# Optimization experiments

Hardware: AMD Instinct MI355X
Metric: run time of the kernel (lower is better)

Reference implementation:

```python
import jax, jax.numpy as jnp
import numpy as np

DIM = 70      # voxel grid side
NE = 6        # element channels
B = 8         # batch
TARGET = 29   # TARGET_NUM in source


def _xavier(key, shape, fan_in, fan_out):
    lim = float(np.sqrt(6.0 / (fan_in + fan_out)))
    return jax.random.uniform(key, shape, jnp.float32, -lim, lim)


def setup_inputs() -> dict:
    key = jax.random.key(0)
    ks = jax.random.split(key, 12)
    # Sparse binary occupancy grid: ~34 atoms per channel per molecule.
    x = (jax.random.uniform(ks[0], (B, NE, DIM, DIM, DIM)) < 1e-4).astype(jnp.float32)
    sigma = 2.0 * jnp.ones((NE,), jnp.float32)
    k3 = 3 * 3 * 3
    conv1_w = _xavier(ks[1], (32, NE, 3, 3, 3), NE * k3, 32 * k3)
    conv2_w = _xavier(ks[2], (64, 32, 3, 3, 3), 32 * k3, 64 * k3)
    conv3_w = _xavier(ks[3], (128, 64, 3, 3, 3), 64 * k3, 128 * k3)
    conv4_w = _xavier(ks[4], (256, 128, 3, 3, 3), 128 * k3, 256 * k3)
    conv1_b = jnp.full((32,), 0.01, jnp.float32)
    conv2_b = jnp.full((64,), 0.01, jnp.float32)
    conv3_b = jnp.full((128,), 0.01, jnp.float32)
    conv4_b = jnp.full((256,), 0.01, jnp.float32)
    fc1_w = _xavier(ks[5], (1024, 2048), 2048, 1024)
    fc1_b = jnp.full((1024,), 0.01, jnp.float32)
    fc2_w = _xavier(ks[6], (TARGET, 1024), 1024, TARGET)
    fc2_b = jax.random.uniform(ks[7], (TARGET,), jnp.float32, -1.0 / 32.0, 1.0 / 32.0)
    return dict(x=x, sigma=sigma,
                conv1_w=conv1_w, conv1_b=conv1_b, conv2_w=conv2_w, conv2_b=conv2_b,
                conv3_w=conv3_w, conv3_b=conv3_b, conv4_w=conv4_w, conv4_b=conv4_b,
                fc1_w=fc1_w, fc1_b=fc1_b, fc2_w=fc2_w, fc2_b=fc2_b)


def _blur(x, sigma):
    # Faithful to source: Gaussian centered at raw voxel INDICES (x0,y0,z0 from
    # nonzero()) but evaluated on SHIFTED coords arange(-dim/2, dim/2).
    # Separable Gaussian -> three 1D contractions instead of per-atom loops.
    coords = jnp.arange(DIM, dtype=jnp.float32) - DIM / 2.0   # -35 .. 34
    idx = jnp.arange(DIM, dtype=jnp.float32)                   # 0 .. 69
    d2 = (coords[:, None] - idx[None, :]) ** 2                 # [70,70]
    G = jnp.exp(-d2[None, :, :] / (2.0 * sigma[:, None, None] ** 2))  # [e,out,in]
    mask = (x != 0).astype(x.dtype)                            # [b,e,i,j,k]
    t = jnp.einsum('beijk,eai->beajk', mask, G)
    t = jnp.einsum('beajk,epj->beapk', t, G)
    cube = jnp.einsum('beapk,eqk->beapq', t, G)                # [b,e,70,70,70]
    return cube


def _conv3d(h, w, b):
    y = jax.lax.conv_general_dilated(h, w, (1, 1, 1), 'VALID',
                                     dimension_numbers=('NCDHW', 'OIDHW', 'NCDHW'))
    return y + b[None, :, None, None, None]


def _pool(h):
    return jax.lax.reduce_window(h, -jnp.inf, jax.lax.max,
                                 (1, 1, 2, 2, 2), (1, 1, 2, 2, 2), 'VALID')


def reference(x, sigma, conv1_w, conv1_b, conv2_w, conv2_b, conv3_w, conv3_b,
              conv4_w, conv4_b, fc1_w, fc1_b, fc2_w, fc2_b):
    h = _blur(x, sigma)
    h = jax.nn.relu(_pool(_conv3d(h, conv1_w, conv1_b)))
    h = jax.nn.relu(_pool(_conv3d(h, conv2_w, conv2_b)))
    h = jax.nn.relu(_pool(_conv3d(h, conv3_w, conv3_b)))
    h = jax.nn.relu(_pool(_conv3d(h, conv4_w, conv4_b)))  # [B,256,2,2,2]
    v = h.reshape(x.shape[0], -1)                          # [B,2048]
    y1 = jax.nn.relu(v @ fc1_w.T + fc1_b)
    y2 = y1 @ fc2_w.T + fc2_b                              # [B,29]
    return y2
```

## Files before the change

### kernel.cpp

```cpp
#include <hip/hip_runtime.h>
#include <hip/hip_bf16.h>

#define DIMV 70
#define NEL 6
#define BATCH 8

typedef unsigned short u16;
typedef unsigned int u32;
typedef __bf16 bf16x8 __attribute__((ext_vector_type(8)));
typedef short short8v __attribute__((ext_vector_type(8)));
typedef float f32x4 __attribute__((ext_vector_type(4)));

__device__ __forceinline__ u16 f2bf(float f) {
  __hip_bfloat16 h = __float2bfloat16(f);
  return __builtin_bit_cast(u16, h);
}
__device__ __forceinline__ float bf2f(u16 u) {
  unsigned int x = ((unsigned int)u) << 16;
  return __builtin_bit_cast(float, x);
}

__global__ __launch_bounds__(256) void k_zero(float* __restrict__ p, int n4) {
  int i = blockIdx.x * 256 + threadIdx.x;
  if (i < n4) ((float4*)p)[i] = make_float4(0.f, 0.f, 0.f, 0.f);
}

__global__ __launch_bounds__(256) void k_scan(const float* __restrict__ x,
                                              int* __restrict__ cnt,
                                              int* __restrict__ lists) {
  const int N4 = (BATCH * NEL * DIMV * DIMV * DIMV) / 4;
  int i = blockIdx.x * 256 + threadIdx.x;
  if (i >= N4) return;
  float4 v = ((const float4*)x)[i];
  int ch = i / 85750;
  int local = 4 * i - ch * 343000;
  float f[4] = {v.x, v.y, v.z, v.w};
#pragma unroll
  for (int k = 0; k < 4; ++k) {
    if (f[k] != 0.f) {
      int slot = atomicAdd(&cnt[ch], 1);
      if (slot < 512) lists[ch * 512 + slot] = local + k;
    }
  }
}

__global__ __launch_bounds__(256) void k_gather(const int* __restrict__ cnt,
                                                const int* __restrict__ lists,
                                                const float* __restrict__ sigma,
                                                u32* __restrict__ cube, int b0) {
  const int z = blockIdx.x;
  const int bl = blockIdx.y / NEL;
  const int e = blockIdx.y % NEL;
  const int chG = (b0 + bl) * NEL + e;
  const int tid = threadIdx.x;
  float sg = sigma[e];
  float inv2s2 = 1.f / (2.f * sg * sg);

  __shared__ int s_n;
  __shared__ int s_idx[512];
  __shared__ float s_wz[512];
  __shared__ float s_wy[32 * 70];
  __shared__ float s_wx[32 * 70];

  if (tid == 0) s_n = 0;
  __syncthreads();
  int n = min(cnt[chG], 512);
  for (int t = tid; t < n; t += 256) {
    int idx = lists[chG * 512 + t];
    int i0 = idx / 4900;
    float d = (float)(z - 35 - i0);
    float wz = expf(-d * d * inv2s2);
    if (wz > 1e-30f) {
      int s = atomicAdd(&s_n, 1);
      s_idx[s] = idx;
      s_wz[s] = wz;
    }
  }
  __syncthreads();
  int m = s_n;

  float acc[20];
#pragma unroll
  for (int k = 0; k < 20; ++k) acc[k] = 0.f;

  for (int t0 = 0; t0 < m; t0 += 32) {
    int tn = min(32, m - t0);
    __syncthreads();
    for (int u = tid; u < tn * 70; u += 256) {
      int t = u / 70, pos = u % 70;
      int idx = s_idx[t0 + t];
      int j0 = (idx / 70) % 70, k0 = idx % 70;
      float dy = (float)(pos - 35 - j0);
      float dx = (float)(pos - 35 - k0);
      s_wy[t * 70 + pos] = s_wz[t0 + t] * expf(-dy * dy * inv2s2);
      s_wx[t * 70 + pos] = expf(-dx * dx * inv2s2);
    }
    __syncthreads();
#pragma unroll
    for (int k = 0; k < 20; ++k) {
      int v = tid + k * 256;
      if (v < 4900) {
        int y = v / 70, xx = v % 70;
        float a = 0.f;
        for (int t = 0; t < tn; ++t)
          a = fmaf(s_wy[t * 70 + y], s_wx[t * 70 + xx], a);
        acc[k] += a;
      }
    }
  }
  size_t base = ((size_t)(bl * NEL + e) * DIMV + z) * 4900;
#pragma unroll
  for (int k = 0; k < 20; ++k) {
    int v = tid + k * 256;
    if (v < 4900) {
      float val = acc[k];
      u16 hi = f2bf(val);
      u16 lo = f2bf(val - bf2f(hi));
      cube[base + v] = ((u32)hi << 16) | (u32)lo;
    }
  }
}

__global__ __launch_bounds__(256) void k_pack_c1d(const float* __restrict__ w,
                                                  u16* __restrict__ Ah,
                                                  u16* __restrict__ Al) {
  int idx = blockIdx.x * 256 + threadIdx.x;
  if (idx >= 32 * 224) return;
  int o = idx / 224, k = idx % 224;
  int kk = k >> 5, r = k & 31;
  int g = r >> 3, e = r & 7;
  int off = 4 * kk + g;
  u16 h = 0, l = 0;
  if (off < 27 && e < 6) {
    float wv = w[(o * 6 + e) * 27 + off];
    u16 hi = f2bf(wv);
    h = hi;
    l = f2bf(wv - bf2f(hi));
  }
  Ah[idx] = h;
  Al[idx] = l;
}

__global__ __launch_bounds__(256) void k_pack_s(const float* __restrict__ w,
                                                u16* __restrict__ A,
                                                int CINL, int COUT) {
  int K2 = CINL * 81;
  int idx = blockIdx.x * 256 + threadIdx.x;
  if (idx >= COUT * K2) return;
  int o = idx / K2, k = idx % K2;
  int kb = k >> 5, r = k & 31;
  int g = r >> 3, e = r & 7;
  int kk = kb % 27;
  int t = kb / 27;
  int snum = CINL >> 5;
  int sub = t % snum, s = t / snum;
  int c = sub * 32 + 8 * g + e;
  float wv = w[(o * CINL + c) * 27 + kk];
  u16 hi = f2bf(wv);
  A[idx] = (s == 2) ? f2bf(wv - bf2f(hi)) : hi;
}

__global__ __launch_bounds__(256) void k_conv1(
    const u16* __restrict__ Ah, const u16* __restrict__ Al,
    const u32* __restrict__ cube, const float* __restrict__ bias,
    float* __restrict__ out, int b0) {
  __shared__ __align__(16) u16 Thi[1120 * 8];
  __shared__ __align__(16) u16 Tlo[1120 * 8];
  const int tid = threadIdx.x;
  const int wave = tid >> 6, lane = tid & 63;
  const int n = lane & 15, g = lane >> 4;
  const int py = blockIdx.x % 34, pz = blockIdx.x / 34;
  const int blb = blockIdx.y, bG = blb + b0;

  u32* thw = (u32*)Thi;
  u32* tlw = (u32*)Tlo;
  for (int i = tid; i < 4480; i += 256) {
    int j = i & 3, pos = i >> 2;
    int xx = pos % 70, line = pos / 70;
    int z = 2 * pz + (line >> 2), y = 2 * py + (line & 3);
    u32 a = 0, b2 = 0;
    if (j < 3) {
      size_t p0 = (((size_t)(blb * 6 + 2 * j) * 70 + z) * 70 + y) * 70 + xx;
      a = cube[p0];
      b2 = cube[p0 + 343000];
    }
    thw[pos * 4 + j] = (a >> 16) | (b2 & 0xFFFF0000u);
    tlw[pos * 4 + j] = (a & 0xFFFFu) | (b2 << 16);
  }
  __syncthreads();

  const int rc = wave;
  f32x4 acc[2][5] = {};
  for (int kk = 0; kk < 7; ++kk) {
    bf16x8 a0[2], a2[2];
#pragma unroll
    for (int mt = 0; mt < 2; ++mt) {
      a0[mt] = __builtin_bit_cast(
          bf16x8, *(const short8v*)(Ah + (size_t)(mt * 16 + n) * 224 + kk * 32 + 8 * g));
      a2[mt] = __builtin_bit_cast(
          bf16x8, *(const short8v*)(Al + (size_t)(mt * 16 + n) * 224 + kk * 32 + 8 * g));
    }
    int off = min(4 * kk + g, 26);
    int dz = off / 9, dy = (off / 3) % 3, dx = off % 3;
    int line = ((rc >> 1) + dz) * 4 + (rc & 1) + dy;
#pragma unroll
    for (int nt = 0; nt < 5; ++nt) {
      int x_in = nt * 16 + n + dx;
      if (x_in > 69) x_in = 69;
      int cell = (line * 70 + x_in) * 8;
      bf16x8 bh = __builtin_bit_cast(bf16x8, *(const short8v*)&Thi[cell]);
      bf16x8 bl = __builtin_bit_cast(bf16x8, *(const short8v*)&Tlo[cell]);
#pragma unroll
      for (int mt = 0; mt < 2; ++mt) {
        acc[mt][nt] = __builtin_amdgcn_mfma_f32_16x16x32_bf16(a0[mt], bh, acc[mt][nt], 0, 0, 0);
        acc[mt][nt] = __builtin_amdgcn_mfma_f32_16x16x32_bf16(a2[mt], bh, acc[mt][nt], 0, 0, 0);
        acc[mt][nt] = __builtin_amdgcn_mfma_f32_16x16x32_bf16(a0[mt], bl, acc[mt][nt], 0, 0, 0);
      }
    }
  }
  __syncthreads();
  float* Pb = (float*)Thi;
#pragma unroll
  for (int mt = 0; mt < 2; ++mt) {
#pragma unroll
    for (int nt = 0; nt < 5; ++nt) {
#pragma unroll
      for (int r = 0; r < 4; ++r) {
        float v = acc[mt][nt][r];
        float v2 = fmaxf(v, __shfl_xor(v, 1));
        int o = mt * 16 + 4 * g + r;
        int px = (nt * 16 + n) >> 1;
        if (!(n & 1) && px < 34) Pb[(wave * 32 + o) * 34 + px] = v2;
      }
    }
  }
  __syncthreads();
  for (int t = tid; t < 1088; t += 256) {
    int o = t / 34, px = t % 34;
    float m = fmaxf(fmaxf(Pb[t], Pb[1088 + t]), fmaxf(Pb[2176 + t], Pb[3264 + t]));
    float rv = fmaxf(m + bias[o], 0.f);
    out[((((size_t)bG * 32 + o) * 34 + pz) * 34 + py) * 34 + px] = rv;
  }
}

template <int CINL, int COUT, int DIN, int WAVES, int MREP, int XT>
__global__ __launch_bounds__(WAVES * 64) void k_conv_s(
    const u16* __restrict__ Apack, const float* __restrict__ in,
    const float* __restrict__ bias, float* __restrict__ out) {
  constexpr int DP = (DIN - 2) / 2;
  constexpr int SNUM = CINL / 32;
  constexpr int K2 = 81 * CINL;
  __shared__ __align__(16) u16 T[16 * DIN * 32];

  const int tid = threadIdx.x;
  const int wave = tid >> 6, lane = tid & 63;
  const int n = lane & 15, g = lane >> 4;
  const int py = blockIdx.x % DP, pz = blockIdx.x / DP;
  const int b = blockIdx.y;

  f32x4 acc[MREP][4][XT] = {};

  for (int ph = 0; ph < 2; ++ph) {
    for (int sub = 0; sub < SNUM; ++sub) {
      if (ph + sub) __syncthreads();
      const int E2 = 16 * DIN * 16;
      for (int i = tid; i < E2; i += WAVES * 64) {
        int xx = i % DIN;
        int t2 = i / DIN;
        int jp = t2 & 15;
        int line = t2 >> 4;
        int z = 2 * pz + (line >> 2), y = 2 * py + (line & 3);
        int c = sub * 32 + 2 * jp;
        size_t base = (((size_t)(b * CINL + c) * DIN + z) * DIN + y) * DIN + xx;
        float v0 = in[base];
        float v1 = in[base + (size_t)DIN * DIN * DIN];
        u16 h0 = f2bf(v0), h1 = f2bf(v1);
        u16 a0 = ph ? f2bf(v0 - bf2f(h0)) : h0;
        u16 a1 = ph ? f2bf(v1 - bf2f(h1)) : h1;
        int byte = (line * DIN + xx) * 64 + (((jp >> 2) ^ ((xx >> 1) & 3)) << 4) + ((jp & 3) << 2);
        *(u32*)((char*)T + byte) = (u32)a0 | ((u32)a1 << 16);
      }
      __syncthreads();
      for (int kk = 0; kk < 27; ++kk) {
        bf16x8 a0[MREP], a2[MREP];
#pragma unroll
        for (int mr = 0; mr < MREP; ++mr) {
          int mtile = wave + WAVES * mr;
          const u16* base = Apack + (size_t)(mtile * 16 + n) * K2 + 8 * g;
          if (ph == 0) {
            a0[mr] = __builtin_bit_cast(
                bf16x8, *(const short8v*)(base + ((0 * SNUM + sub) * 27 + kk) * 32));
            a2[mr] = __builtin_bit_cast(
                bf16x8, *(const short8v*)(base + ((2 * SNUM + sub) * 27 + kk) * 32));
          } else {
            a0[mr] = __builtin_bit_cast(
                bf16x8, *(const short8v*)(base + ((1 * SNUM + sub) * 27 + kk) * 32));
          }
        }
        int dz = kk / 9, dy = (kk / 3) % 3, dx = kk % 3;
#pragma unroll
        for (int rc = 0; rc < 4; ++rc) {
          int line = ((rc >> 1) + dz) * 4 + (rc & 1) + dy;
#pragma unroll
          for (int nt = 0; nt < XT; ++nt) {
            int x_in = nt * 16 + n + dx;
            if (x_in > DIN - 1) x_in = DIN - 1;
            int byte = (line * DIN + x_in) * 64 + ((g ^ ((x_in >> 1) & 3)) << 4);
            bf16x8 bfr = __builtin_bit_cast(bf16x8, *(const short8v*)((const char*)T + byte));
#pragma unroll
            for (int mr = 0; mr < MREP; ++mr) {
              acc[mr][rc][nt] =
                  __builtin_amdgcn_mfma_f32_16x16x32_bf16(a0[mr], bfr, acc[mr][rc][nt], 0, 0, 0);
              if (ph == 0)
                acc[mr][rc][nt] = __builtin_amdgcn_mfma_f32_16x16x32_bf16(
                    a2[mr], bfr, acc[mr][rc][nt], 0, 0, 0);
            }
          }
        }
      }
    }
  }
#pragma unroll
  for (int mr = 0; mr < MREP; ++mr) {
    int mtile = wave + WAVES * mr;
#pragma unroll
    for (int nt = 0; nt < XT; ++nt) {
#pragma unroll
      for (int r = 0; r < 4; ++r) {
        float v = fmaxf(fmaxf(acc[mr][0][nt][r], acc[mr][1][nt][r]),
                        fmaxf(acc[mr][2][nt][r], acc[mr][3][nt][r]));
        float v2 = fmaxf(v, __shfl_xor(v, 1));
        int o = mtile * 16 + 4 * g + r;
        int px = (nt * 16 + n) >> 1;
        if (!(n & 1) && px < DP) {
          float rv = fmaxf(v2 + bias[o], 0.f);
          out[((((size_t)b * COUT + o) * DP + pz) * DP + py) * DP + px] = rv;
        }
      }
    }
  }
}

__global__ __launch_bounds__(512) void k_conv4ks(
    const u16* __restrict__ Apack, const float* __restrict__ in,
    float* __restrict__ P) {
  __shared__ __align__(16) u16 T[343 * 32];
  const int tid = threadIdx.x;
  const int wave = tid >> 6, lane = tid & 63;
  const int n = lane & 15, g = lane >> 4;
  const int q = blockIdx.x;
  const int third = q >> 3;
  const int r8 = q & 7;
  const int ph = r8 >> 2, sub = r8 & 3;
  const int b = blockIdx.y;

  for (int i = tid; i < 343 * 16; i += 512) {
    int jp = i & 15, pos = i >> 4;
    int c = sub * 32 + 2 * jp;
    const float* src = in + (size_t)(b * 128 + c) * 343 + pos;
    float v0 = src[0];
    float v1 = src[343];
    u16 h0 = f2bf(v0), h1 = f2bf(v1);
    u16 a0 = ph ? f2bf(v0 - bf2f(h0)) : h0;
    u16 a1 = ph ? f2bf(v1 - bf2f(h1)) : h1;
    int byte = pos * 64 + (((jp >> 2) ^ (pos & 3)) << 4) + ((jp & 3) << 2);
    *(u32*)((char*)T + byte) = (u32)a0 | ((u32)a1 << 16);
  }
  __syncthreads();

  f32x4 acc[2][4] = {};
  const int ys = n >> 2, xo = n & 3;
  for (int t = 0; t < 9; ++t) {
    int kk = third * 9 + t;
    int dz = kk / 9, dy = (kk / 3) % 3, dx = kk % 3;
    bf16x8 a0[2], a2[2];
#pragma unroll
    for (int mr = 0; mr < 2; ++mr) {
      int mtile = wave + 8 * mr;
      const u16* base = Apack + (size_t)(mtile * 16 + n) * 10368 + 8 * g;
      if (ph == 0) {
        a0[mr] = __builtin_bit_cast(
            bf16x8, *(const short8v*)(base + ((0 * 4 + sub) * 27 + kk) * 32));
        a2[mr] = __builtin_bit_cast(
            bf16x8, *(const short8v*)(base + ((2 * 4 + sub) * 27 + kk) * 32));
      } else {
        a0[mr] = __builtin_bit_cast(
            bf16x8, *(const short8v*)(base + ((1 * 4 + sub) * 27 + kk) * 32));
      }
    }
    int ybase = (ys + dy) * 7 + xo + dx;
#pragma unroll
    for (int zr = 0; zr < 4; ++zr) {
      int pos = (zr + dz) * 49 + ybase;
      int byte = pos * 64 + ((g ^ (pos & 3)) << 4);
      bf16x8 bfr = __builtin_bit_cast(bf16x8, *(const short8v*)((const char*)T + byte));
#pragma unroll
      for (int mr = 0; mr < 2; ++mr) {
        acc[mr][zr] = __builtin_amdgcn_mfma_f32_16x16x32_bf16(a0[mr], bfr, acc[mr][zr], 0, 0, 0);
        if (ph == 0)
          acc[mr][zr] = __builtin_amdgcn_mfma_f32_16x16x32_bf16(a2[mr], bfr, acc[mr][zr], 0, 0, 0);
      }
    }
  }
  float* Pq = P + (size_t)(q * 8 + b) * 16384;
#pragma unroll
  for (int mr = 0; mr < 2; ++mr) {
    int mtile = wave + 8 * mr;
#pragma unroll
    for (int zr = 0; zr < 4; ++zr) {
#pragma unroll
      for (int r = 0; r < 4; ++r) {
        int o = mtile * 16 + 4 * g + r;
        Pq[o * 64 + zr * 16 + n] = acc[mr][zr][r];
      }
    }
  }
}

__global__ __launch_bounds__(256) void k_fin4(const float* __restrict__ P,
                                              const float* __restrict__ bias,
                                              float* __restrict__ h4) {
  int t = blockIdx.x * 256 + threadIdx.x;
  if (t >= 16384) return;
  int w = t & 7;
  int o = (t >> 3) & 255;
  int b = t >> 11;
  int pd = w >> 2, p2 = (w >> 1) & 1, pw = w & 1;
  float m = -1e30f;
#pragma unroll
  for (int dz = 0; dz < 2; ++dz)
#pragma unroll
    for (int dy = 0; dy < 2; ++dy)
#pragma unroll
      for (int dx = 0; dx < 2; ++dx) {
        int pos = (2 * pd + dz) * 16 + (2 * p2 + dy) * 4 + (2 * pw + dx);
        float s = 0.f;
        for (int q = 0; q < 24; ++q)
          s += P[(size_t)(q * 8 + b) * 16384 + o * 64 + pos];
        m = fmaxf(m, s);
      }
  h4[(size_t)b * 2048 + o * 8 + w] = fmaxf(m + bias[o], 0.f);
}

__global__ __launch_bounds__(256) void k_fc1(const float* __restrict__ v,
                                             const float* __restrict__ W,
                                             const float* __restrict__ bias,
                                             float* __restrict__ y) {
  int o = blockIdx.x;
  int tid = threadIdx.x;
  int wave = tid >> 6, lane = tid & 63;
  __shared__ float red[4][8];
  float acc[8] = {};
  const float* wp = W + (size_t)o * 2048 + wave * 512;
  const float* vp = v + wave * 512;
  for (int k = lane; k < 512; k += 64) {
    float wv = wp[k];
#pragma unroll
    for (int bb = 0; bb < 8; ++bb)
      acc[bb] = fmaf(vp[bb * 2048 + k], wv, acc[bb]);
  }
#pragma unroll
  for (int off = 32; off; off >>= 1)
#pragma unroll
    for (int bb = 0; bb < 8; ++bb) acc[bb] += __shfl_xor(acc[bb], off);
  if (lane == 0) {
#pragma unroll
    for (int bb = 0; bb < 8; ++bb) red[wave][bb] = acc[bb];
  }
  __syncthreads();
  if (tid < 8) {
    float s = red[0][tid] + red[1][tid] + red[2][tid] + red[3][tid];
    y[tid * 1024 + o] = fmaxf(s + bias[o], 0.f);
  }
}

__global__ __launch_bounds__(64) void k_fc2(const float* __restrict__ v,
                                            const float* __restrict__ W,
                                            const float* __restrict__ bias,
                                            float* __restrict__ y) {
  int o = blockIdx.x;
  int lane = threadIdx.x;
  float acc[8] = {};
  for (int k = lane; k < 1024; k += 64) {
    float wv = W[o * 1024 + k];
#pragma unroll
    for (int bb = 0; bb < 8; ++bb)
      acc[bb] = fmaf(v[bb * 1024 + k], wv, acc[bb]);
  }
#pragma unroll
  for (int off = 32; off; off >>= 1)
#pragma unroll
    for (int bb = 0; bb < 8; ++bb) acc[bb] += __shfl_xor(acc[bb], off);
  if (lane == 0) {
    float bo = bias[o];
#pragma unroll
    for (int bb = 0; bb < 8; ++bb) y[bb * 29 + o] = acc[bb] + bo;
  }
}

extern "C" void kernel_launch(void* const* d_in, const int* in_sizes, int n_in,
                              void* d_out, int out_size, void* d_ws, size_t ws_size,
                              hipStream_t stream) {
  const float* x   = (const float*)d_in[0];
  const float* sig = (const float*)d_in[1];
  const float* w1  = (const float*)d_in[2];
  const float* b1  = (const float*)d_in[3];
  const float* w2  = (const float*)d_in[4];
  const float* b2  = (const float*)d_in[5];
  const float* w3  = (const float*)d_in[6];
  const float* b3  = (const float*)d_in[7];
  const float* w4  = (const float*)d_in[8];
  const float* b4  = (const float*)d_in[9];
  const float* fw1 = (const float*)d_in[10];
  const float* fb1 = (const float*)d_in[11];
  const float* fw2 = (const float*)d_in[12];
  const float* fb2 = (const float*)d_in[13];

  char* ws = (char*)d_ws;
  u32*   cube4 = (u32*)(ws + 0);
  float* P     = (float*)(ws + 0);
  float* h1    = (float*)(ws + 32928000);
  u16*   ah1   = (u16*)(ws + 73200000);
  u16*   al1   = (u16*)(ws + 73250000);
  u16*   ap2   = (u16*)(ws + 73300000);
  u16*   ap3   = (u16*)(ws + 73700000);
  u16*   ap4   = (u16*)(ws + 75100000);
  float* h2    = (float*)(ws + 80500000);
  float* h3    = (float*)(ws + 89000000);
  float* h4    = (float*)(ws + 90500000);
  float* y1    = (float*)(ws + 90600000);
  int*   cnt   = (int*)(ws + 90700000);
  int*   lists = (int*)(ws + 90701024);

  k_pack_c1d<<<(32 * 224 + 255) / 256, 256, 0, stream>>>(w1, ah1, al1);
  k_pack_s<<<(64 * 2592 + 255) / 256, 256, 0, stream>>>(w2, ap2, 32, 64);
  k_pack_s<<<(128 * 5184 + 255) / 256, 256, 0, stream>>>(w3, ap3, 64, 128);
  k_pack_s<<<(256 * 10368 + 255) / 256, 256, 0, stream>>>(w4, ap4, 128, 256);

  k_zero<<<1, 256, 0, stream>>>((float*)cnt, 12);
  const int N4 = (BATCH * NEL * DIMV * DIMV * DIMV) / 4;
  k_scan<<<(N4 + 255) / 256, 256, 0, stream>>>(x, cnt, lists);

  for (int half = 0; half < 2; ++half) {
    int b0 = 4 * half;
    k_gather<<<dim3(DIMV, 4 * NEL), 256, 0, stream>>>(cnt, lists, sig, cube4, b0);
    k_conv1<<<dim3(34 * 34, 4), 256, 0, stream>>>(ah1, al1, cube4, b1, h1, b0);
  }

  k_conv_s<32,  64, 34, 4, 1, 2><<<dim3(16 * 16, 8), 256, 0, stream>>>(ap2, h1, b2, h2);
  k_conv_s<64, 128, 16, 8, 1, 1><<<dim3(7 * 7, 8),   512, 0, stream>>>(ap3, h2, b3, h3);

  k_conv4ks<<<dim3(24, 8), 512, 0, stream>>>(ap4, h3, P);
  k_fin4<<<64, 256, 0, stream>>>(P, b4, h4);

  k_fc1<<<1024, 256, 0, stream>>>(h4, fw1, fb1, y1);
  k_fc2<<<29, 64, 0, stream>>>(y1, fw2, fb2, (float*)d_out);
}
```

Before: 550.5 us.

## Merge split-bf16 passes into one staging pass with hi and lo LDS tiles

The conv2/conv3 kernel used to run two passes over the input: one staging the bf16 high parts and one staging the low residuals, reloading and reconverting the activations from global memory each time. It now converts once, stores both hi and lo tiles in shared memory, and issues all three MFMAs per fragment in a single loop. This halves global activation reads, tile conversions and barriers, but doubles LDS use per block, which can reduce occupancy. The MREP parameter is dropped because it was always 1.

```diff
diff --git a/kernel.cpp b/kernel.cpp
--- a/kernel.cpp
+++ b/kernel.cpp
@@ -243,14 +243,15 @@
   }
 }
 
-template <int CINL, int COUT, int DIN, int WAVES, int MREP, int XT>
-__global__ __launch_bounds__(WAVES * 64) void k_conv_s(
+template <int CINL, int COUT, int DIN, int WAVES, int XT>
+__global__ __launch_bounds__(WAVES * 64) void k_conv_m(
     const u16* __restrict__ Apack, const float* __restrict__ in,
     const float* __restrict__ bias, float* __restrict__ out) {
   constexpr int DP = (DIN - 2) / 2;
   constexpr int SNUM = CINL / 32;
   constexpr int K2 = 81 * CINL;
-  __shared__ __align__(16) u16 T[16 * DIN * 32];
+  __shared__ __align__(16) u16 Thi[16 * DIN * 32];
+  __shared__ __align__(16) u16 Tlo[16 * DIN * 32];
 
   const int tid = threadIdx.x;
   const int wave = tid >> 6, lane = tid & 63;
@@ -258,84 +259,65 @@
   const int py = blockIdx.x % DP, pz = blockIdx.x / DP;
   const int b = blockIdx.y;
 
-  f32x4 acc[MREP][4][XT] = {};
-
-  for (int ph = 0; ph < 2; ++ph) {
-    for (int sub = 0; sub < SNUM; ++sub) {
-      if (ph + sub) __syncthreads();
-      const int E2 = 16 * DIN * 16;
-      for (int i = tid; i < E2; i += WAVES * 64) {
-        int xx = i % DIN;
-        int t2 = i / DIN;
-        int jp = t2 & 15;
-        int line = t2 >> 4;
-        int z = 2 * pz + (line >> 2), y = 2 * py + (line & 3);
-        int c = sub * 32 + 2 * jp;
-        size_t base = (((size_t)(b * CINL + c) * DIN + z) * DIN + y) * DIN + xx;
-        float v0 = in[base];
-        float v1 = in[base + (size_t)DIN * DIN * DIN];
-        u16 h0 = f2bf(v0), h1 = f2bf(v1);
-        u16 a0 = ph ? f2bf(v0 - bf2f(h0)) : h0;
-        u16 a1 = ph ? f2bf(v1 - bf2f(h1)) : h1;
-        int byte = (line * DIN + xx) * 64 + (((jp >> 2) ^ ((xx >> 1) & 3)) << 4) + ((jp & 3) << 2);
-        *(u32*)((char*)T + byte) = (u32)a0 | ((u32)a1 << 16);
-      }
-      __syncthreads();
-      for (int kk = 0; kk < 27; ++kk) {
-        bf16x8 a0[MREP], a2[MREP];
-#pragma unroll
-        for (int mr = 0; mr < MREP; ++mr) {
-          int mtile = wave + WAVES * mr;
-          const u16* base = Apack + (size_t)(mtile * 16 + n) * K2 + 8 * g;
-          if (ph == 0) {
-            a0[mr] = __builtin_bit_cast(
-                bf16x8, *(const short8v*)(base + ((0 * SNUM + sub) * 27 + kk) * 32));
-            a2[mr] = __builtin_bit_cast(
-                bf16x8, *(const short8v*)(base + ((2 * SNUM + sub) * 27 + kk) * 32));
-          } else {
-            a0[mr] = __builtin_bit_cast(
-                bf16x8, *(const short8v*)(base + ((1 * SNUM + sub) * 27 + kk) * 32));
-          }
+  f32x4 acc[4][XT] = {};
+
+  for (int sub = 0; sub < SNUM; ++sub) {
+    if (sub) __syncthreads();
+    const int E2 = 16 * DIN * 16;
+    for (int i = tid; i < E2; i += WAVES * 64) {
+      int xx = i % DIN;
+      int t2 = i / DIN;
+      int jp = t2 & 15;
+      int line = t2 >> 4;
+      int z = 2 * pz + (line >> 2), y = 2 * py + (line & 3);
+      int c = sub * 32 + 2 * jp;
+      size_t base = (((size_t)(b * CINL + c) * DIN + z) * DIN + y) * DIN + xx;
+      float v0 = in[base];
+      float v1 = in[base + (size_t)DIN * DIN * DIN];
+      u16 h0 = f2bf(v0), h1 = f2bf(v1);
+      u16 l0 = f2bf(v0 - bf2f(h0));
+      u16 l1 = f2bf(v1 - bf2f(h1));
+      int byte = (line * DIN + xx) * 64 + (((jp >> 2) ^ ((xx >> 1) & 3)) << 4) + ((jp & 3) << 2);
+      *(u32*)((char*)Thi + byte) = (u32)h0 | ((u32)h1 << 16);
+      *(u32*)((char*)Tlo + byte) = (u32)l0 | ((u32)l1 << 16);
+    }
+    __syncthreads();
+    for (int kk = 0; kk < 27; ++kk) {
+      const u16* abase = Apack + (size_t)(wave * 16 + n) * K2 + 8 * g;
+      bf16x8 a0 = __builtin_bit_cast(
+          bf16x8, *(const short8v*)(abase + ((0 * SNUM + sub) * 27 + kk) * 32));
+      bf16x8 a2 = __builtin_bit_cast(
+          bf16x8, *(const short8v*)(abase + ((2 * SNUM + sub) * 27 + kk) * 32));
+      int dz = kk / 9, dy = (kk / 3) % 3, dx = kk % 3;
+#pragma unroll
+      for (int rc = 0; rc < 4; ++rc) {
+        int line = ((rc >> 1) + dz) * 4 + (rc & 1) + dy;
+#pragma unroll
+        for (int nt = 0; nt < XT; ++nt) {
+          int x_in = nt * 16 + n + dx;
+          if (x_in > DIN - 1) x_in = DIN - 1;
+          int byte = (line * DIN + x_in) * 64 + ((g ^ ((x_in >> 1) & 3)) << 4);
+          bf16x8 bh = __builtin_bit_cast(bf16x8, *(const short8v*)((const char*)Thi + byte));
+          bf16x8 bl = __builtin_bit_cast(bf16x8, *(const short8v*)((const char*)Tlo + byte));
+          acc[rc][nt] = __builtin_amdgcn_mfma_f32_16x16x32_bf16(a0, bh, acc[rc][nt], 0, 0, 0);
+          acc[rc][nt] = __builtin_amdgcn_mfma_f32_16x16x32_bf16(a2, bh, acc[rc][nt], 0, 0, 0);
+          acc[rc][nt] = __builtin_amdgcn_mfma_f32_16x16x32_bf16(a0, bl, acc[rc][nt], 0, 0, 0);
         }
-        int dz = kk / 9, dy = (kk / 3) % 3, dx = kk % 3;
-#pragma unroll
-        for (int rc = 0; rc < 4; ++rc) {
-          int line = ((rc >> 1) + dz) * 4 + (rc & 1) + dy;
-#pragma unroll
-          for (int nt = 0; nt < XT; ++nt) {
-            int x_in = nt * 16 + n + dx;
-            if (x_in > DIN - 1) x_in = DIN - 1;
-            int byte = (line * DIN + x_in) * 64 + ((g ^ ((x_in >> 1) & 3)) << 4);
-            bf16x8 bfr = __builtin_bit_cast(bf16x8, *(const short8v*)((const char*)T + byte));
-#pragma unroll
-            for (int mr = 0; mr < MREP; ++mr) {
-              acc[mr][rc][nt] =
-                  __builtin_amdgcn_mfma_f32_16x16x32_bf16(a0[mr], bfr, acc[mr][rc][nt], 0, 0, 0);
-              if (ph == 0)
-                acc[mr][rc][nt] = __builtin_amdgcn_mfma_f32_16x16x32_bf16(
-                    a2[mr], bfr, acc[mr][rc][nt], 0, 0, 0);
-            }
-          }
-        }
-      }
-    }
-  }
-#pragma unroll
-  for (int mr = 0; mr < MREP; ++mr) {
-    int mtile = wave + WAVES * mr;
-#pragma unroll
-    for (int nt = 0; nt < XT; ++nt) {
-#pragma unroll
-      for (int r = 0; r < 4; ++r) {
-        float v = fmaxf(fmaxf(acc[mr][0][nt][r], acc[mr][1][nt][r]),
-                        fmaxf(acc[mr][2][nt][r], acc[mr][3][nt][r]));
-        float v2 = fmaxf(v, __shfl_xor(v, 1));
-        int o = mtile * 16 + 4 * g + r;
-        int px = (nt * 16 + n) >> 1;
-        if (!(n & 1) && px < DP) {
-          float rv = fmaxf(v2 + bias[o], 0.f);
-          out[((((size_t)b * COUT + o) * DP + pz) * DP + py) * DP + px] = rv;
-        }
+      }
+    }
+  }
+#pragma unroll
+  for (int nt = 0; nt < XT; ++nt) {
+#pragma unroll
+    for (int r = 0; r < 4; ++r) {
+      float v = fmaxf(fmaxf(acc[0][nt][r], acc[1][nt][r]),
+                      fmaxf(acc[2][nt][r], acc[3][nt][r]));
+      float v2 = fmaxf(v, __shfl_xor(v, 1));
+      int o = wave * 16 + 4 * g + r;
+      int px = (nt * 16 + n) >> 1;
+      if (!(n & 1) && px < DP) {
+        float rv = fmaxf(v2 + bias[o], 0.f);
+        out[((((size_t)b * COUT + o) * DP + pz) * DP + py) * DP + px] = rv;
       }
     }
   }
@@ -547,8 +529,8 @@
     k_conv1<<<dim3(34 * 34, 4), 256, 0, stream>>>(ah1, al1, cube4, b1, h1, b0);
   }
 
-  k_conv_s<32,  64, 34, 4, 1, 2><<<dim3(16 * 16, 8), 256, 0, stream>>>(ap2, h1, b2, h2);
-  k_conv_s<64, 128, 16, 8, 1, 1><<<dim3(7 * 7, 8),   512, 0, stream>>>(ap3, h2, b3, h3);
+  k_conv_m<32,  64, 34, 4, 2><<<dim3(16 * 16, 8), 256, 0, stream>>>(ap2, h1, b2, h2);
+  k_conv_m<64, 128, 16, 8, 1><<<dim3(7 * 7, 8),   512, 0, stream>>>(ap3, h2, b3, h3);
 
   k_conv4ks<<<dim3(24, 8), 512, 0, stream>>>(ap4, h3, P);
   k_fin4<<<64, 256, 0, stream>>>(P, b4, h4);
```

Result: faster. 529.7 us (-3.8%).
